# Kernel tuning notes

Measured on AMD Instinct MI355X. Metric: run time of the kernel, lower is better.

The kernel has to match this reference:

```python
import jax, jax.numpy as jnp
import numpy as np

B, SEQ, DIM = 4, 2048, 2048
NH, HD = 16, 128            # head_dim = dim // n_head
HID = 5632                  # int(2*(4*dim)/3) rounded up to multiple_of=256
EPS = 1e-5
THETA = 500000.0


def setup_inputs() -> dict:
    key = jax.random.key(0)
    ks = jax.random.split(key, 9)
    s = 0.02  # init scale keeps activations/logits well-conditioned
    x = jax.random.normal(ks[0], (B, SEQ, DIM), jnp.float32)
    wq = jax.random.normal(ks[1], (DIM, DIM), jnp.float32) * s
    wk = jax.random.normal(ks[2], (DIM, DIM), jnp.float32) * s
    wv = jax.random.normal(ks[3], (DIM, DIM), jnp.float32) * s
    wo = jax.random.normal(ks[4], (DIM, DIM), jnp.float32) * s
    w1 = jax.random.normal(ks[5], (DIM, HID), jnp.float32) * s
    w2 = jax.random.normal(ks[6], (HID, DIM), jnp.float32) * s
    w3 = jax.random.normal(ks[7], (DIM, HID), jnp.float32) * s
    attn_norm_w = jnp.ones((DIM,), jnp.float32)
    ffn_norm_w = jnp.ones((DIM,), jnp.float32)
    # RoPE tables (real/imag of freqs_cis), [seq, head_dim//2]
    inv = 1.0 / (THETA ** (jnp.arange(0, HD, 2, dtype=jnp.float32) / HD))
    ang = jnp.arange(SEQ, dtype=jnp.float32)[:, None] * inv[None, :]
    return dict(x=x, wq=wq, wk=wk, wv=wv, wo=wo, w1=w1, w2=w2, w3=w3,
                attn_norm_w=attn_norm_w, ffn_norm_w=ffn_norm_w,
                freqs_cos=jnp.cos(ang), freqs_sin=jnp.sin(ang))


def rmsnorm(x, w, eps=EPS):
    return x * jax.lax.rsqrt(jnp.mean(x * x, axis=-1, keepdims=True) + eps) * w


def rope(x, cos, sin):
    # x: [b, s, h, d]; pairs (d0,d1),(d2,d3),... treated as complex, multiplied by e^{i*ang}
    a, b = x[..., 0::2], x[..., 1::2]
    c = cos[None, :, None, :]
    s = sin[None, :, None, :]
    return jnp.stack([a * c - b * s, a * s + b * c], axis=-1).reshape(x.shape)


def block(x, wq, wk, wv, wo, w1, w2, w3, attn_norm_w, ffn_norm_w, freqs_cos, freqs_sin):
    b, s, d = x.shape
    # --- attention sublayer ---
    hn = rmsnorm(x, attn_norm_w)
    q = (hn @ wq).reshape(b, s, NH, HD)
    k = (hn @ wk).reshape(b, s, NH, HD)
    v = (hn @ wv).reshape(b, s, NH, HD)
    q = rope(q, freqs_cos, freqs_sin)
    k = rope(k, freqs_cos, freqs_sin)
    scores = jnp.einsum('bqhd,bkhd->bhqk', q, k) / np.float32(np.sqrt(HD))
    mask = jnp.triu(jnp.full((s, s), -jnp.inf, dtype=scores.dtype), k=1)
    p = jax.nn.softmax(scores + mask, axis=-1)
    attn = jnp.einsum('bhqk,bkhd->bqhd', p, v).reshape(b, s, d) @ wo
    h = x + attn
    # --- SwiGLU FFN sublayer ---
    fn = rmsnorm(h, ffn_norm_w)
    ffn = (jax.nn.silu(fn @ w1) * (fn @ w3)) @ w2
    return h + ffn


def reference(x, wq, wk, wv, wo, w1, w2, w3, attn_norm_w, ffn_norm_w, freqs_cos, freqs_sin):
    return block(x, wq, wk, wv, wo, w1, w2, w3, attn_norm_w, ffn_norm_w, freqs_cos, freqs_sin)
```

## Files before the change

### kernel.cpp

```cpp
#include <hip/hip_runtime.h>
#include <stdint.h>

#define DIMV 2048
#define SEQV 2048
#define NHV 16
#define HDV 128
#define HIDV 5632
#define NROWS 8192
#define LDP 6144

typedef short bf16x8 __attribute__((ext_vector_type(8)));
typedef float f32x4 __attribute__((ext_vector_type(4)));
typedef unsigned short u16x8 __attribute__((ext_vector_type(8)));

#define GLD16(src, dst) __builtin_amdgcn_global_load_lds( \
    (const __attribute__((address_space(1))) unsigned int*)(src), \
    (__attribute__((address_space(3))) unsigned int*)(dst), 16, 0, 0)

__device__ __forceinline__ float bf2f(unsigned short u){
  union { unsigned u; float f; } x; x.u = ((unsigned)u) << 16; return x.f;
}
__device__ __forceinline__ unsigned short f2bf(float f){
  union { float f; unsigned u; } x; x.f = f;
  unsigned r = x.u + 0x7fffu + ((x.u >> 16) & 1u);
  return (unsigned short)(r >> 16);
}

__global__ void transpose_cast(const float* __restrict__ in, unsigned short* __restrict__ out,
                               int R, int C){
  __shared__ alignas(16) unsigned short tile[32][33];
  int c0 = blockIdx.x * 32, r0 = blockIdx.y * 32;
  int tx = threadIdx.x, ty = threadIdx.y;
#pragma unroll
  for (int i = 0; i < 32; i += 8)
    tile[ty + i][tx] = f2bf(in[(long)(r0 + ty + i) * C + (c0 + tx)]);
  __syncthreads();
#pragma unroll
  for (int i = 0; i < 32; i += 8)
    out[(long)(c0 + ty + i) * R + (r0 + tx)] = tile[tx][ty + i];
}

__global__ void transpose_v(const unsigned short* __restrict__ packed, unsigned short* __restrict__ vt){
  __shared__ alignas(16) unsigned short tile[32][33];
  int bh = blockIdx.z;
  int b = bh >> 4, h = bh & 15;
  int d0 = blockIdx.y * 32, s0 = blockIdx.x * 32;
  int tx = threadIdx.x, ty = threadIdx.y;
  const unsigned short* src = packed + (long)b * SEQV * LDP + 4096 + (long)h * HDV;
  unsigned short* dst = vt + (long)bh * HDV * SEQV;
#pragma unroll
  for (int i = 0; i < 32; i += 8)
    tile[ty + i][tx] = src[(long)(s0 + ty + i) * LDP + d0 + tx];
  __syncthreads();
#pragma unroll
  for (int i = 0; i < 32; i += 8)
    dst[(long)(d0 + ty + i) * SEQV + s0 + tx] = tile[tx][ty + i];
}

__global__ __launch_bounds__(256) void rmsnorm_k(const float* __restrict__ x,
                                                 const float* __restrict__ w,
                                                 unsigned short* __restrict__ out){
  int row = blockIdx.x, t = threadIdx.x;
  const float* xr = x + (long)row * DIMV;
  float4 v0 = ((const float4*)xr)[t * 2];
  float4 v1 = ((const float4*)xr)[t * 2 + 1];
  float ss = v0.x*v0.x + v0.y*v0.y + v0.z*v0.z + v0.w*v0.w
           + v1.x*v1.x + v1.y*v1.y + v1.z*v1.z + v1.w*v1.w;
#pragma unroll
  for (int off = 32; off; off >>= 1) ss += __shfl_down(ss, off);
  __shared__ float red[4];
  if ((t & 63) == 0) red[t >> 6] = ss;
  __syncthreads();
  float tot = red[0] + red[1] + red[2] + red[3];
  float sc = rsqrtf(tot * (1.0f / DIMV) + 1e-5f);
  const float* wr = w + t * 8;
  float vv[8] = {v0.x, v0.y, v0.z, v0.w, v1.x, v1.y, v1.z, v1.w};
  u16x8 o;
#pragma unroll
  for (int e = 0; e < 8; e++) o[e] = f2bf(vv[e] * sc * wr[e]);
  *(u16x8*)(out + (long)row * DIMV + t * 8) = o;
}

template <int MODE>
__global__ __launch_bounds__(512, 2) void gemm256(const unsigned short* __restrict__ A, int lda,
                                                  const unsigned short* __restrict__ Bt,
                                                  unsigned short* __restrict__ Cb,
                                                  float* __restrict__ Cf,
                                                  const float* __restrict__ resid,
                                                  int ldc, int M, int N, int K){
  __shared__ alignas(16) unsigned short As[2][256 * 64];
  __shared__ alignas(16) unsigned short Bs[2][256 * 64];
  int m0 = blockIdx.y * 256, n0 = blockIdx.x * 256;
  int tid = threadIdx.x, w = tid >> 6, l = tid & 63;
  int wm = w >> 2, wn = w & 3;
  int l15 = l & 15, l4 = l >> 4;
  int sr8 = l >> 3, sl = l & 7;
  int nt = K / 64;

  f32x4 acc[8][4];
#pragma unroll
  for (int i = 0; i < 8; i++)
#pragma unroll
    for (int j = 0; j < 4; j++) acc[i][j] = (f32x4){0.f, 0.f, 0.f, 0.f};

#define GSTAGE(Gp, ld_, r0_, slab) { \
    _Pragma("unroll") \
    for (int r = 0; r < 2; r++){ \
      int row = (r * 8 + w) * 8 + sr8; \
      int cs = sl ^ (row & 7); \
      GLD16((Gp) + (long)((r0_) + row) * (ld_) + cs * 8, (slab) + (r * 8 + w) * 512); \
    } }
#define STAGE_A(tt, half) { int _t = (tt); if (_t < nt) GSTAGE(A + _t * 64, lda, m0 + (half) * 128, &As[_t & 1][(half) * 8192]) }
#define STAGE_B(tt, half) { int _t = (tt); if (_t < nt) GSTAGE(Bt + _t * 64, K, n0 + (half) * 128, &Bs[_t & 1][(half) * 8192]) }
#define LDA8(mi, ks) (*(const bf16x8*)(&As[bi][(wm * 128 + (mi) * 16 + l15) * 64 + (((ks) * 4 + l4) ^ (l15 & 7)) * 8]))
#define LDB8(ni, ks) (*(const bf16x8*)(&Bs[bi][(wn * 64 + (ni) * 16 + l15) * 64 + (((ks) * 4 + l4) ^ (l15 & 7)) * 8]))

  STAGE_A(0, 0); STAGE_A(0, 1); STAGE_B(0, 0); STAGE_B(0, 1);
  STAGE_A(1, 0); STAGE_B(1, 0); STAGE_B(1, 1);
  asm volatile("s_waitcnt vmcnt(6)" ::: "memory");
  __syncthreads();

  for (int t = 0; t < nt; t++){
    int bi = t & 1;
    bf16x8 af[8][2], bf0[2][2], bf1[2][2];
#pragma unroll
    for (int mi = 0; mi < 8; mi++){ af[mi][0] = LDA8(mi, 0); af[mi][1] = LDA8(mi, 1); }
#pragma unroll
    for (int ni = 0; ni < 2; ni++){ bf0[ni][0] = LDB8(ni, 0); bf0[ni][1] = LDB8(ni, 1); }
    STAGE_A(t + 1, 1);
    __builtin_amdgcn_s_barrier();
    asm volatile("s_waitcnt lgkmcnt(0)" ::: "memory");
    __builtin_amdgcn_sched_barrier(0);
    __builtin_amdgcn_s_setprio(1);
#pragma unroll
    for (int mi = 0; mi < 4; mi++)
#pragma unroll
      for (int ni = 0; ni < 2; ni++)
#pragma unroll
        for (int ks = 0; ks < 2; ks++)
          acc[mi][ni] = __builtin_amdgcn_mfma_f32_16x16x32_bf16(af[mi][ks], bf0[ni][ks], acc[mi][ni], 0, 0, 0);
    __builtin_amdgcn_s_setprio(0);
    __builtin_amdgcn_s_barrier();
#pragma unroll
    for (int ni = 0; ni < 2; ni++){ bf1[ni][0] = LDB8(ni + 2, 0); bf1[ni][1] = LDB8(ni + 2, 1); }
    STAGE_A(t + 2, 0);
    __builtin_amdgcn_s_barrier();
    asm volatile("s_waitcnt lgkmcnt(0)" ::: "memory");
    __builtin_amdgcn_sched_barrier(0);
    __builtin_amdgcn_s_setprio(1);
#pragma unroll
    for (int mi = 4; mi < 8; mi++)
#pragma unroll
      for (int ni = 0; ni < 2; ni++)
#pragma unroll
        for (int ks = 0; ks < 2; ks++)
          acc[mi][ni] = __builtin_amdgcn_mfma_f32_16x16x32_bf16(af[mi][ks], bf0[ni][ks], acc[mi][ni], 0, 0, 0);
    __builtin_amdgcn_s_setprio(0);
    __builtin_amdgcn_s_barrier();
    STAGE_B(t + 2, 0);
    __builtin_amdgcn_s_barrier();
    __builtin_amdgcn_s_setprio(1);
#pragma unroll
    for (int mi = 0; mi < 4; mi++)
#pragma unroll
      for (int ni = 0; ni < 2; ni++)
#pragma unroll
        for (int ks = 0; ks < 2; ks++)
          acc[mi][ni + 2] = __builtin_amdgcn_mfma_f32_16x16x32_bf16(af[mi][ks], bf1[ni][ks], acc[mi][ni + 2], 0, 0, 0);
    __builtin_amdgcn_s_setprio(0);
    __builtin_amdgcn_s_barrier();
    STAGE_B(t + 2, 1);
    __builtin_amdgcn_s_barrier();
    __builtin_amdgcn_s_setprio(1);
#pragma unroll
    for (int mi = 4; mi < 8; mi++)
#pragma unroll
      for (int ni = 0; ni < 2; ni++)
#pragma unroll
        for (int ks = 0; ks < 2; ks++)
          acc[mi][ni + 2] = __builtin_amdgcn_mfma_f32_16x16x32_bf16(af[mi][ks], bf1[ni][ks], acc[mi][ni + 2], 0, 0, 0);
    __builtin_amdgcn_s_setprio(0);
    if (t + 2 < nt) asm volatile("s_waitcnt vmcnt(6)" ::: "memory");
    else            asm volatile("s_waitcnt vmcnt(0)" ::: "memory");
    __builtin_amdgcn_s_barrier();
  }
#undef GSTAGE
#undef STAGE_A
#undef STAGE_B
#undef LDA8
#undef LDB8

#pragma unroll
  for (int mi = 0; mi < 8; mi++)
#pragma unroll
    for (int ni = 0; ni < 4; ni++)
#pragma unroll
      for (int r = 0; r < 4; r++){
        int row = m0 + wm * 128 + mi * 16 + l4 * 4 + r;
        int col = n0 + wn * 64 + ni * 16 + l15;
        long idx = (long)row * ldc + col;
        float v = acc[mi][ni][r];
        if (MODE == 0) Cb[idx] = f2bf(v);
        else           Cf[idx] = v + resid[idx];
      }
}

__global__ __launch_bounds__(512, 2) void ffn13_256(const unsigned short* __restrict__ A,
                                                    const unsigned short* __restrict__ B1t,
                                                    const unsigned short* __restrict__ B3t,
                                                    unsigned short* __restrict__ G,
                                                    int M, int N, int K){
  __shared__ alignas(16) unsigned short As[2][256 * 64];
  __shared__ alignas(16) unsigned short B1s[2][128 * 64];
  __shared__ alignas(16) unsigned short B3s[2][128 * 64];
  int m0 = blockIdx.y * 256, n0 = blockIdx.x * 128;
  int tid = threadIdx.x, w = tid >> 6, l = tid & 63;
  int wm = w >> 2, wn = w & 3;
  int l15 = l & 15, l4 = l >> 4;
  int sr8 = l >> 3, sl = l & 7;
  int nt = K / 64;

  f32x4 acc1[8][2], acc3[8][2];
#pragma unroll
  for (int i = 0; i < 8; i++)
#pragma unroll
    for (int j = 0; j < 2; j++){ acc1[i][j] = (f32x4){0.f,0.f,0.f,0.f}; acc3[i][j] = (f32x4){0.f,0.f,0.f,0.f}; }

#define GSTAGE(Gp, ld_, r0_, slab) { \
    _Pragma("unroll") \
    for (int r = 0; r < 2; r++){ \
      int row = (r * 8 + w) * 8 + sr8; \
      int cs = sl ^ (row & 7); \
      GLD16((Gp) + (long)((r0_) + row) * (ld_) + cs * 8, (slab) + (r * 8 + w) * 512); \
    } }
#define STAGE_A(tt, half) { int _t = (tt); if (_t < nt) GSTAGE(A + _t * 64, K, m0 + (half) * 128, &As[_t & 1][(half) * 8192]) }
#define STAGE_B1(tt) { int _t = (tt); if (_t < nt) GSTAGE(B1t + _t * 64, K, n0, &B1s[_t & 1][0]) }
#define STAGE_B3(tt) { int _t = (tt); if (_t < nt) GSTAGE(B3t + _t * 64, K, n0, &B3s[_t & 1][0]) }
#define LDA8(mi, ks) (*(const bf16x8*)(&As[bi][(wm * 128 + (mi) * 16 + l15) * 64 + (((ks) * 4 + l4) ^ (l15 & 7)) * 8]))
#define LDB18(ni, ks) (*(const bf16x8*)(&B1s[bi][(wn * 32 + (ni) * 16 + l15) * 64 + (((ks) * 4 + l4) ^ (l15 & 7)) * 8]))
#define LDB38(ni, ks) (*(const bf16x8*)(&B3s[bi][(wn * 32 + (ni) * 16 + l15) * 64 + (((ks) * 4 + l4) ^ (l15 & 7)) * 8]))

  STAGE_A(0, 0); STAGE_A(0, 1); STAGE_B1(0); STAGE_B3(0);
  STAGE_A(1, 0); STAGE_B1(1); STAGE_B3(1);
  asm volatile("s_waitcnt vmcnt(6)" ::: "memory");
  __syncthreads();

  for (int t = 0; t < nt; t++){
    int bi = t & 1;
    bf16x8 af[8][2], b1f[2][2], b3f[2][2];
#pragma unroll
    for (int mi = 0; mi < 8; mi++){ af[mi][0] = LDA8(mi, 0); af[mi][1] = LDA8(mi, 1); }
#pragma unroll
    for (int ni = 0; ni < 2; ni++){ b1f[ni][0] = LDB18(ni, 0); b1f[ni][1] = LDB18(ni, 1); }
    STAGE_A(t + 1, 1);
    __builtin_amdgcn_s_barrier();
    asm volatile("s_waitcnt lgkmcnt(0)" ::: "memory");
    __builtin_amdgcn_sched_barrier(0);
    __builtin_amdgcn_s_setprio(1);
#pragma unroll
    for (int mi = 0; mi < 4; mi++)
#pragma unroll
      for (int ni = 0; ni < 2; ni++)
#pragma unroll
        for (int ks = 0; ks < 2; ks++)
          acc1[mi][ni] = __builtin_amdgcn_mfma_f32_16x16x32_bf16(af[mi][ks], b1f[ni][ks], acc1[mi][ni], 0, 0, 0);
    __builtin_amdgcn_s_setprio(0);
    __builtin_amdgcn_s_barrier();
#pragma unroll
    for (int ni = 0; ni < 2; ni++){ b3f[ni][0] = LDB38(ni, 0); b3f[ni][1] = LDB38(ni, 1); }
    STAGE_A(t + 2, 0);
    __builtin_amdgcn_s_barrier();
    asm volatile("s_waitcnt lgkmcnt(0)" ::: "memory");
    __builtin_amdgcn_sched_barrier(0);
    __builtin_amdgcn_s_setprio(1);
#pragma unroll
    for (int mi = 4; mi < 8; mi++)
#pragma unroll
      for (int ni = 0; ni < 2; ni++)
#pragma unroll
        for (int ks = 0; ks < 2; ks++)
          acc1[mi][ni] = __builtin_amdgcn_mfma_f32_16x16x32_bf16(af[mi][ks], b1f[ni][ks], acc1[mi][ni], 0, 0, 0);
    __builtin_amdgcn_s_setprio(0);
    __builtin_amdgcn_s_barrier();
    STAGE_B1(t + 2);
    __builtin_amdgcn_s_barrier();
    __builtin_amdgcn_s_setprio(1);
#pragma unroll
    for (int mi = 0; mi < 4; mi++)
#pragma unroll
      for (int ni = 0; ni < 2; ni++)
#pragma unroll
        for (int ks = 0; ks < 2; ks++)
          acc3[mi][ni] = __builtin_amdgcn_mfma_f32_16x16x32_bf16(af[mi][ks], b3f[ni][ks], acc3[mi][ni], 0, 0, 0);
    __builtin_amdgcn_s_setprio(0);
    __builtin_amdgcn_s_barrier();
    STAGE_B3(t + 2);
    __builtin_amdgcn_s_barrier();
    __builtin_amdgcn_s_setprio(1);
#pragma unroll
    for (int mi = 4; mi < 8; mi++)
#pragma unroll
      for (int ni = 0; ni < 2; ni++)
#pragma unroll
        for (int ks = 0; ks < 2; ks++)
          acc3[mi][ni] = __builtin_amdgcn_mfma_f32_16x16x32_bf16(af[mi][ks], b3f[ni][ks], acc3[mi][ni], 0, 0, 0);
    __builtin_amdgcn_s_setprio(0);
    if (t + 2 < nt) asm volatile("s_waitcnt vmcnt(6)" ::: "memory");
    else            asm volatile("s_waitcnt vmcnt(0)" ::: "memory");
    __builtin_amdgcn_s_barrier();
  }
#undef GSTAGE
#undef STAGE_A
#undef STAGE_B1
#undef STAGE_B3
#undef LDA8
#undef LDB18
#undef LDB38

#pragma unroll
  for (int mi = 0; mi < 8; mi++)
#pragma unroll
    for (int ni = 0; ni < 2; ni++)
#pragma unroll
      for (int r = 0; r < 4; r++){
        int row = m0 + wm * 128 + mi * 16 + l4 * 4 + r;
        int col = n0 + wn * 32 + ni * 16 + l15;
        float a = acc1[mi][ni][r];
        float si = a * (1.f / (1.f + __expf(-a)));
        G[(long)row * N + col] = f2bf(si * acc3[mi][ni][r]);
      }
}

__global__ __launch_bounds__(256) void rope_k(unsigned short* __restrict__ p,
                                              const float* __restrict__ cosT,
                                              const float* __restrict__ sinT,
                                              float qscale){
  long idx = (long)blockIdx.x * 256 + threadIdx.x;
  int i = (int)(idx & 63);
  long t = idx >> 6;
  int h = (int)(t & 15);
  long row = t >> 4;
  int s = (int)(row & (SEQV - 1));
  float c = cosT[s * 64 + i], sn = sinT[s * 64 + i];
  long base = row * LDP + h * HDV + 2 * i;
  unsigned pq = *(unsigned*)(p + base);
  float a = bf2f((unsigned short)(pq & 0xffff)), b = bf2f((unsigned short)(pq >> 16));
  float ra = (a * c - b * sn) * qscale, rb = (a * sn + b * c) * qscale;
  *(unsigned*)(p + base) = (unsigned)f2bf(ra) | ((unsigned)f2bf(rb) << 16);
  unsigned pk = *(unsigned*)(p + base + 2048);
  a = bf2f((unsigned short)(pk & 0xffff)); b = bf2f((unsigned short)(pk >> 16));
  ra = a * c - b * sn; rb = a * sn + b * c;
  *(unsigned*)(p + base + 2048) = (unsigned)f2bf(ra) | ((unsigned)f2bf(rb) << 16);
}

__global__ __launch_bounds__(256) void attn_k(unsigned short* __restrict__ p,
                                              const unsigned short* __restrict__ vt){
  __shared__ alignas(16) unsigned short Ks[2][64 * 128];
  __shared__ alignas(16) unsigned short Vs[2][128 * 64];
  __shared__ alignas(16) unsigned short Ps[4][16 * 64];
  int qt = (gridDim.x - 1) - blockIdx.x;
  int bh = blockIdx.y;
  int b = bh >> 4, h = bh & 15;
  int tid = threadIdx.x, w = tid >> 6, l = tid & 63;
  int l15 = l & 15, l4 = l >> 4;
  int qrow0 = qt * 64 + w * 16;
  long baseQ = (long)b * SEQV * LDP + (long)h * HDV;
  long baseV = (long)bh * HDV * SEQV;

  bf16x8 qf[4];
#pragma unroll
  for (int dc = 0; dc < 4; dc++)
    qf[dc] = *(const bf16x8*)(p + baseQ + (long)(qrow0 + l15) * LDP + dc * 32 + l4 * 8);

  f32x4 acc[8];
#pragma unroll
  for (int df = 0; df < 8; df++) acc[df] = (f32x4){0.f, 0.f, 0.f, 0.f};
  float mOld[4], lsum[4];
#pragma unroll
  for (int r = 0; r < 4; r++){ mOld[r] = -1e30f; lsum[r] = 0.f; }

#define ATTN_STAGE(buf, kt) {                                                       \
    int k0 = (kt) * 64;                                                             \
    _Pragma("unroll")                                                               \
    for (int i = 0; i < 4; i++){                                                    \
      int row = w * 16 + i * 4 + (l >> 4);                                          \
      int slot = (l & 15) ^ (row & 7);                                              \
      GLD16(p + baseQ + 2048 + (long)(k0 + row) * LDP + slot * 8,                   \
            Ks[buf] + (w * 16 + i * 4) * 128);                                      \
    }                                                                               \
    _Pragma("unroll")                                                               \
    for (int i = 0; i < 4; i++){                                                    \
      int row = w * 32 + i * 8 + (l >> 3);                                          \
      int slot = (l & 7) ^ (row & 7);                                               \
      GLD16(vt + baseV + (long)row * SEQV + k0 + slot * 8,                          \
            Vs[buf] + (w * 32 + i * 8) * 64);                                       \
    } }

  int ntile = qt + 1;
  ATTN_STAGE(0, 0);
  asm volatile("s_waitcnt vmcnt(0)" ::: "memory");
  __syncthreads();
  int cur = 0;
  for (int tki = 0; tki < ntile; tki++){
    int k0 = tki * 64;
    if (tki + 1 < ntile) ATTN_STAGE(cur ^ 1, tki + 1);

    float s[4][4];
    __builtin_amdgcn_s_setprio(1);
#pragma unroll
    for (int kf = 0; kf < 4; kf++){
      f32x4 sf = (f32x4){0.f, 0.f, 0.f, 0.f};
#pragma unroll
      for (int dc = 0; dc < 4; dc++){
        bf16x8 kb = *(const bf16x8*)(Ks[cur] + (kf * 16 + l15) * 128 + (((dc * 4 + l4) ^ (l15 & 7)) * 8));
        sf = __builtin_amdgcn_mfma_f32_16x16x32_bf16(qf[dc], kb, sf, 0, 0, 0);
      }
      int key = k0 + kf * 16 + l15;
#pragma unroll
      for (int r = 0; r < 4; r++){
        int rowi = qrow0 + l4 * 4 + r;
        s[kf][r] = (key <= rowi) ? sf[r] : -1e30f;
      }
    }
    __builtin_amdgcn_s_setprio(0);
    float scale[4];
#pragma unroll
    for (int r = 0; r < 4; r++){
      float vmax = fmaxf(fmaxf(s[0][r], s[1][r]), fmaxf(s[2][r], s[3][r]));
      for (int mm = 8; mm; mm >>= 1) vmax = fmaxf(vmax, __shfl_xor(vmax, mm));
      float mNew = fmaxf(mOld[r], vmax);
      scale[r] = __expf(mOld[r] - mNew);
      float ps = 0.f;
#pragma unroll
      for (int kf = 0; kf < 4; kf++){
        float pp = __expf(s[kf][r] - mNew);
        s[kf][r] = pp;
        ps += pp;
      }
      for (int mm = 8; mm; mm >>= 1) ps += __shfl_xor(ps, mm);
      lsum[r] = lsum[r] * scale[r] + ps;
      mOld[r] = mNew;
    }
#pragma unroll
    for (int df = 0; df < 8; df++)
#pragma unroll
      for (int r = 0; r < 4; r++) acc[df][r] *= scale[r];
#pragma unroll
    for (int kf = 0; kf < 4; kf++)
#pragma unroll
      for (int r = 0; r < 4; r++){
        int row = l4 * 4 + r;
        int sidx = row * 64 + (((((kf * 16 + l15) * 2)) ^ ((row & 7) << 4)) >> 1);
        Ps[w][sidx] = f2bf(s[kf][r]);
      }
    __builtin_amdgcn_s_setprio(1);
#pragma unroll
    for (int kc = 0; kc < 2; kc++){
      bf16x8 pa = *(const bf16x8*)(Ps[w] + l15 * 64 + (((kc * 64 + l4 * 16) ^ ((l15 & 7) << 4)) >> 1));
#pragma unroll
      for (int df = 0; df < 8; df++){
        bf16x8 vb = *(const bf16x8*)(Vs[cur] + (df * 16 + l15) * 64 + (((kc * 4 + l4) ^ (l15 & 7)) * 8));
        acc[df] = __builtin_amdgcn_mfma_f32_16x16x32_bf16(pa, vb, acc[df], 0, 0, 0);
      }
    }
    __builtin_amdgcn_s_setprio(0);
    asm volatile("s_waitcnt vmcnt(0)" ::: "memory");
    __syncthreads();
    cur ^= 1;
  }
#pragma unroll
  for (int df = 0; df < 8; df++)
#pragma unroll
    for (int r = 0; r < 4; r++){
      int rows = qrow0 + l4 * 4 + r;
      p[baseQ + (long)rows * LDP + df * 16 + l15] = f2bf(acc[df][r] / lsum[r]);
    }
#undef ATTN_STAGE
}

extern "C" void kernel_launch(void* const* d_in, const int* in_sizes, int n_in,
                              void* d_out, int out_size, void* d_ws, size_t ws_size,
                              hipStream_t stream){
  const float* x    = (const float*)d_in[0];
  const float* wq   = (const float*)d_in[1];
  const float* wk   = (const float*)d_in[2];
  const float* wv   = (const float*)d_in[3];
  const float* wo   = (const float*)d_in[4];
  const float* w1   = (const float*)d_in[5];
  const float* w2   = (const float*)d_in[6];
  const float* w3   = (const float*)d_in[7];
  const float* anw  = (const float*)d_in[8];
  const float* fnw  = (const float*)d_in[9];
  const float* fcos = (const float*)d_in[10];
  const float* fsin = (const float*)d_in[11];

  char* ws = (char*)d_ws;
  size_t off = 0;
  auto alloc = [&](size_t bytes) -> void* {
    void* p = ws + off;
    off += (bytes + 255) & ~(size_t)255;
    return p;
  };
  const size_t SQ = (size_t)DIMV * DIMV * 2;
  const size_t SW = (size_t)DIMV * HIDV * 2;
  const size_t SA = (size_t)NROWS * DIMV * 2;
  const size_t SP = (size_t)NROWS * LDP * 2;

  unsigned short* wqT = (unsigned short*)alloc(SQ);
  unsigned short* wkT = (unsigned short*)alloc(SQ);
  unsigned short* wvT = (unsigned short*)alloc(SQ);
  unsigned short* woT = (unsigned short*)alloc(SQ);
  unsigned short* w1T = (unsigned short*)alloc(SW);
  unsigned short* w3T = (unsigned short*)alloc(SW);
  unsigned short* w2T = (unsigned short*)alloc(SW);
  unsigned short* hn  = (unsigned short*)alloc(SA);
  unsigned short* pk  = (unsigned short*)alloc(SP);
  unsigned short* vtb = hn;
  unsigned short* g   = pk;
  float* hf = (float*)d_out;
  (void)ws_size; (void)in_sizes; (void)n_in; (void)out_size;
  (void)wkT; (void)wvT;

  dim3 tb(32, 8);
  transpose_cast<<<dim3(DIMV/32, DIMV/32), tb, 0, stream>>>(wq, wqT, DIMV, DIMV);
  transpose_cast<<<dim3(DIMV/32, DIMV/32), tb, 0, stream>>>(wk, wkT, DIMV, DIMV);
  transpose_cast<<<dim3(DIMV/32, DIMV/32), tb, 0, stream>>>(wv, wvT, DIMV, DIMV);
  transpose_cast<<<dim3(DIMV/32, DIMV/32), tb, 0, stream>>>(wo, woT, DIMV, DIMV);
  transpose_cast<<<dim3(HIDV/32, DIMV/32), tb, 0, stream>>>(w1, w1T, DIMV, HIDV);
  transpose_cast<<<dim3(HIDV/32, DIMV/32), tb, 0, stream>>>(w3, w3T, DIMV, HIDV);
  transpose_cast<<<dim3(DIMV/32, HIDV/32), tb, 0, stream>>>(w2, w2T, HIDV, DIMV);

  rmsnorm_k<<<NROWS, 256, 0, stream>>>(x, anw, hn);

  gemm256<0><<<dim3(LDP/256, NROWS/256), 512, 0, stream>>>(hn, DIMV, wqT, pk, nullptr, nullptr, LDP, NROWS, LDP, DIMV);

  rope_k<<<(NROWS * NHV * 64) / 256, 256, 0, stream>>>(pk, fcos, fsin, 0.08838834764831845f);

  transpose_v<<<dim3(SEQV/32, HDV/32, 4 * NHV), tb, 0, stream>>>(pk, vtb);

  attn_k<<<dim3(SEQV/64, 4 * NHV), 256, 0, stream>>>(pk, vtb);

  gemm256<1><<<dim3(DIMV/256, NROWS/256), 512, 0, stream>>>(pk, LDP, woT, nullptr, hf, x, DIMV, NROWS, DIMV, DIMV);

  rmsnorm_k<<<NROWS, 256, 0, stream>>>(hf, fnw, hn);

  ffn13_256<<<dim3(HIDV/128, NROWS/256), 512, 0, stream>>>(hn, w1T, w3T, g, NROWS, HIDV, DIMV);

  gemm256<1><<<dim3(DIMV/256, NROWS/256), 512, 0, stream>>>(g, HIDV, w2T, nullptr, hf, (const float*)hf, DIMV, NROWS, DIMV, HIDV);
}
```

Measured before the change: 1.276 ms.

## Software-pipeline LDS fragment reads against MFMA quadrants in GEMM kernels

In both the generic 256x256 GEMM and the fused FFN w1/w3 kernel, the A fragments are split into two halves and the B fragments into two pairs. Each half is loaded from LDS just before the MFMA quadrant that needs it. The first quadrant's fragments for the next k-tile are prefetched while the last quadrant's MFMAs run, and the explicit lgkmcnt(0) waits are removed. The goal is to hide LDS read latency behind matrix-core work instead of stalling before each compute phase. This adds more scheduling barriers, and correctness now relies on the compiler inserting the LDS waits.

```diff
diff --git a/kernel.cpp b/kernel.cpp
--- a/kernel.cpp
+++ b/kernel.cpp
@@ -80,6 +80,9 @@
   for (int e = 0; e < 8; e++) o[e] = f2bf(vv[e] * sc * wr[e]);
   *(u16x8*)(out + (long)row * DIMV + t * 8) = o;
 }
+
+#define SCHEDB() __builtin_amdgcn_sched_barrier(0)
+#define SBAR()   __builtin_amdgcn_s_barrier()
 
 template <int MODE>
 __global__ __launch_bounds__(512, 2) void gemm256(const unsigned short* __restrict__ A, int lda,
@@ -112,83 +115,79 @@
     } }
 #define STAGE_A(tt, half) { int _t = (tt); if (_t < nt) GSTAGE(A + _t * 64, lda, m0 + (half) * 128, &As[_t & 1][(half) * 8192]) }
 #define STAGE_B(tt, half) { int _t = (tt); if (_t < nt) GSTAGE(Bt + _t * 64, K, n0 + (half) * 128, &Bs[_t & 1][(half) * 8192]) }
-#define LDA8(mi, ks) (*(const bf16x8*)(&As[bi][(wm * 128 + (mi) * 16 + l15) * 64 + (((ks) * 4 + l4) ^ (l15 & 7)) * 8]))
-#define LDB8(ni, ks) (*(const bf16x8*)(&Bs[bi][(wn * 64 + (ni) * 16 + l15) * 64 + (((ks) * 4 + l4) ^ (l15 & 7)) * 8]))
+#define LDA8(bb, mi, ks) (*(const bf16x8*)(&As[bb][(wm * 128 + (mi) * 16 + l15) * 64 + (((ks) * 4 + l4) ^ (l15 & 7)) * 8]))
+#define LDB8(bb, ni, ks) (*(const bf16x8*)(&Bs[bb][(wn * 64 + (ni) * 16 + l15) * 64 + (((ks) * 4 + l4) ^ (l15 & 7)) * 8]))
+#define Q_MFMA(AF, BF, MOFF, NOFF) { \
+    _Pragma("unroll") \
+    for (int mi = 0; mi < 4; mi++) \
+      _Pragma("unroll") \
+      for (int ni = 0; ni < 2; ni++) \
+        _Pragma("unroll") \
+        for (int ks = 0; ks < 2; ks++) \
+          acc[mi + (MOFF)][ni + (NOFF)] = __builtin_amdgcn_mfma_f32_16x16x32_bf16(AF[mi][ks], BF[ni][ks], acc[mi + (MOFF)][ni + (NOFF)], 0, 0, 0); }
+
+  bf16x8 a03[4][2], a47[4][2], b01[2][2], b23[2][2];
 
   STAGE_A(0, 0); STAGE_A(0, 1); STAGE_B(0, 0); STAGE_B(0, 1);
   STAGE_A(1, 0); STAGE_B(1, 0); STAGE_B(1, 1);
   asm volatile("s_waitcnt vmcnt(6)" ::: "memory");
-  __syncthreads();
+  SBAR();
+  SCHEDB();
+#pragma unroll
+  for (int mi = 0; mi < 4; mi++){ a03[mi][0] = LDA8(0, mi, 0); a03[mi][1] = LDA8(0, mi, 1); }
+#pragma unroll
+  for (int ni = 0; ni < 2; ni++){ b01[ni][0] = LDB8(0, ni, 0); b01[ni][1] = LDB8(0, ni, 1); }
+  SCHEDB();
 
   for (int t = 0; t < nt; t++){
     int bi = t & 1;
-    bf16x8 af[8][2], bf0[2][2], bf1[2][2];
-#pragma unroll
-    for (int mi = 0; mi < 8; mi++){ af[mi][0] = LDA8(mi, 0); af[mi][1] = LDA8(mi, 1); }
-#pragma unroll
-    for (int ni = 0; ni < 2; ni++){ bf0[ni][0] = LDB8(ni, 0); bf0[ni][1] = LDB8(ni, 1); }
+#pragma unroll
+    for (int mi = 0; mi < 4; mi++){ a47[mi][0] = LDA8(bi, mi + 4, 0); a47[mi][1] = LDA8(bi, mi + 4, 1); }
     STAGE_A(t + 1, 1);
-    __builtin_amdgcn_s_barrier();
-    asm volatile("s_waitcnt lgkmcnt(0)" ::: "memory");
-    __builtin_amdgcn_sched_barrier(0);
-    __builtin_amdgcn_s_setprio(1);
-#pragma unroll
-    for (int mi = 0; mi < 4; mi++)
-#pragma unroll
-      for (int ni = 0; ni < 2; ni++)
-#pragma unroll
-        for (int ks = 0; ks < 2; ks++)
-          acc[mi][ni] = __builtin_amdgcn_mfma_f32_16x16x32_bf16(af[mi][ks], bf0[ni][ks], acc[mi][ni], 0, 0, 0);
-    __builtin_amdgcn_s_setprio(0);
-    __builtin_amdgcn_s_barrier();
-#pragma unroll
-    for (int ni = 0; ni < 2; ni++){ bf1[ni][0] = LDB8(ni + 2, 0); bf1[ni][1] = LDB8(ni + 2, 1); }
+    SCHEDB(); SBAR(); SCHEDB();
+    __builtin_amdgcn_s_setprio(1);
+    Q_MFMA(a03, b01, 0, 0);
+    __builtin_amdgcn_s_setprio(0);
+    SCHEDB(); SBAR();
+#pragma unroll
+    for (int ni = 0; ni < 2; ni++){ b23[ni][0] = LDB8(bi, ni + 2, 0); b23[ni][1] = LDB8(bi, ni + 2, 1); }
     STAGE_A(t + 2, 0);
-    __builtin_amdgcn_s_barrier();
-    asm volatile("s_waitcnt lgkmcnt(0)" ::: "memory");
-    __builtin_amdgcn_sched_barrier(0);
-    __builtin_amdgcn_s_setprio(1);
-#pragma unroll
-    for (int mi = 4; mi < 8; mi++)
-#pragma unroll
-      for (int ni = 0; ni < 2; ni++)
-#pragma unroll
-        for (int ks = 0; ks < 2; ks++)
-          acc[mi][ni] = __builtin_amdgcn_mfma_f32_16x16x32_bf16(af[mi][ks], bf0[ni][ks], acc[mi][ni], 0, 0, 0);
-    __builtin_amdgcn_s_setprio(0);
-    __builtin_amdgcn_s_barrier();
+    SCHEDB(); SBAR(); SCHEDB();
+    __builtin_amdgcn_s_setprio(1);
+    Q_MFMA(a47, b01, 4, 0);
+    __builtin_amdgcn_s_setprio(0);
+    SCHEDB(); SBAR();
     STAGE_B(t + 2, 0);
-    __builtin_amdgcn_s_barrier();
-    __builtin_amdgcn_s_setprio(1);
-#pragma unroll
-    for (int mi = 0; mi < 4; mi++)
-#pragma unroll
-      for (int ni = 0; ni < 2; ni++)
-#pragma unroll
-        for (int ks = 0; ks < 2; ks++)
-          acc[mi][ni + 2] = __builtin_amdgcn_mfma_f32_16x16x32_bf16(af[mi][ks], bf1[ni][ks], acc[mi][ni + 2], 0, 0, 0);
-    __builtin_amdgcn_s_setprio(0);
-    __builtin_amdgcn_s_barrier();
+    SCHEDB(); SBAR(); SCHEDB();
+    __builtin_amdgcn_s_setprio(1);
+    Q_MFMA(a03, b23, 0, 2);
+    __builtin_amdgcn_s_setprio(0);
+    SCHEDB(); SBAR();
     STAGE_B(t + 2, 1);
-    __builtin_amdgcn_s_barrier();
-    __builtin_amdgcn_s_setprio(1);
-#pragma unroll
-    for (int mi = 4; mi < 8; mi++)
-#pragma unroll
-      for (int ni = 0; ni < 2; ni++)
-#pragma unroll
-        for (int ks = 0; ks < 2; ks++)
-          acc[mi][ni + 2] = __builtin_amdgcn_mfma_f32_16x16x32_bf16(af[mi][ks], bf1[ni][ks], acc[mi][ni + 2], 0, 0, 0);
-    __builtin_amdgcn_s_setprio(0);
+    SCHEDB();
     if (t + 2 < nt) asm volatile("s_waitcnt vmcnt(6)" ::: "memory");
     else            asm volatile("s_waitcnt vmcnt(0)" ::: "memory");
-    __builtin_amdgcn_s_barrier();
+    SBAR();
+    SCHEDB();
+    if (t + 1 < nt){
+      int bj = bi ^ 1;
+#pragma unroll
+      for (int mi = 0; mi < 4; mi++){ a03[mi][0] = LDA8(bj, mi, 0); a03[mi][1] = LDA8(bj, mi, 1); }
+#pragma unroll
+      for (int ni = 0; ni < 2; ni++){ b01[ni][0] = LDB8(bj, ni, 0); b01[ni][1] = LDB8(bj, ni, 1); }
+    }
+    SCHEDB();
+    __builtin_amdgcn_s_setprio(1);
+    Q_MFMA(a47, b23, 4, 2);
+    __builtin_amdgcn_s_setprio(0);
+    SCHEDB(); SBAR();
   }
 #undef GSTAGE
 #undef STAGE_A
 #undef STAGE_B
 #undef LDA8
 #undef LDB8
+#undef Q_MFMA
 
 #pragma unroll
   for (int mi = 0; mi < 8; mi++)
@@ -236,78 +235,73 @@
 #define STAGE_A(tt, half) { int _t = (tt); if (_t < nt) GSTAGE(A + _t * 64, K, m0 + (half) * 128, &As[_t & 1][(half) * 8192]) }
 #define STAGE_B1(tt) { int _t = (tt); if (_t < nt) GSTAGE(B1t + _t * 64, K, n0, &B1s[_t & 1][0]) }
 #define STAGE_B3(tt) { int _t = (tt); if (_t < nt) GSTAGE(B3t + _t * 64, K, n0, &B3s[_t & 1][0]) }
-#define LDA8(mi, ks) (*(const bf16x8*)(&As[bi][(wm * 128 + (mi) * 16 + l15) * 64 + (((ks) * 4 + l4) ^ (l15 & 7)) * 8]))
-#define LDB18(ni, ks) (*(const bf16x8*)(&B1s[bi][(wn * 32 + (ni) * 16 + l15) * 64 + (((ks) * 4 + l4) ^ (l15 & 7)) * 8]))
-#define LDB38(ni, ks) (*(const bf16x8*)(&B3s[bi][(wn * 32 + (ni) * 16 + l15) * 64 + (((ks) * 4 + l4) ^ (l15 & 7)) * 8]))
+#define LDA8(bb, mi, ks) (*(const bf16x8*)(&As[bb][(wm * 128 + (mi) * 16 + l15) * 64 + (((ks) * 4 + l4) ^ (l15 & 7)) * 8]))
+#define LDB18(bb, ni, ks) (*(const bf16x8*)(&B1s[bb][(wn * 32 + (ni) * 16 + l15) * 64 + (((ks) * 4 + l4) ^ (l15 & 7)) * 8]))
+#define LDB38(bb, ni, ks) (*(const bf16x8*)(&B3s[bb][(wn * 32 + (ni) * 16 + l15) * 64 + (((ks) * 4 + l4) ^ (l15 & 7)) * 8]))
+#define Q_MFMA(AF, BF, ACC, MOFF) { \
+    _Pragma("unroll") \
+    for (int mi = 0; mi < 4; mi++) \
+      _Pragma("unroll") \
+      for (int ni = 0; ni < 2; ni++) \
+        _Pragma("unroll") \
+        for (int ks = 0; ks < 2; ks++) \
+          ACC[mi + (MOFF)][ni] = __builtin_amdgcn_mfma_f32_16x16x32_bf16(AF[mi][ks], BF[ni][ks], ACC[mi + (MOFF)][ni], 0, 0, 0); }
+
+  bf16x8 a03[4][2], a47[4][2], b1f[2][2], b3f[2][2];
 
   STAGE_A(0, 0); STAGE_A(0, 1); STAGE_B1(0); STAGE_B3(0);
   STAGE_A(1, 0); STAGE_B1(1); STAGE_B3(1);
   asm volatile("s_waitcnt vmcnt(6)" ::: "memory");
-  __syncthreads();
+  SBAR();
+  SCHEDB();
+#pragma unroll
+  for (int mi = 0; mi < 4; mi++){ a03[mi][0] = LDA8(0, mi, 0); a03[mi][1] = LDA8(0, mi, 1); }
+#pragma unroll
+  for (int ni = 0; ni < 2; ni++){ b1f[ni][0] = LDB18(0, ni, 0); b1f[ni][1] = LDB18(0, ni, 1); }
+  SCHEDB();
 
   for (int t = 0; t < nt; t++){
     int bi = t & 1;
-    bf16x8 af[8][2], b1f[2][2], b3f[2][2];
-#pragma unroll
-    for (int mi = 0; mi < 8; mi++){ af[mi][0] = LDA8(mi, 0); af[mi][1] = LDA8(mi, 1); }
-#pragma unroll
-    for (int ni = 0; ni < 2; ni++){ b1f[ni][0] = LDB18(ni, 0); b1f[ni][1] = LDB18(ni, 1); }
+#pragma unroll
+    for (int mi = 0; mi < 4; mi++){ a47[mi][0] = LDA8(bi, mi + 4, 0); a47[mi][1] = LDA8(bi, mi + 4, 1); }
     STAGE_A(t + 1, 1);
-    __builtin_amdgcn_s_barrier();
-    asm volatile("s_waitcnt lgkmcnt(0)" ::: "memory");
-    __builtin_amdgcn_sched_barrier(0);
-    __builtin_amdgcn_s_setprio(1);
-#pragma unroll
-    for (int mi = 0; mi < 4; mi++)
-#pragma unroll
-      for (int ni = 0; ni < 2; ni++)
-#pragma unroll
-        for (int ks = 0; ks < 2; ks++)
-          acc1[mi][ni] = __builtin_amdgcn_mfma_f32_16x16x32_bf16(af[mi][ks], b1f[ni][ks], acc1[mi][ni], 0, 0, 0);
-    __builtin_amdgcn_s_setprio(0);
-    __builtin_amdgcn_s_barrier();
-#pragma unroll
-    for (int ni = 0; ni < 2; ni++){ b3f[ni][0] = LDB38(ni, 0); b3f[ni][1] = LDB38(ni, 1); }
+    SCHEDB(); SBAR(); SCHEDB();
+    __builtin_amdgcn_s_setprio(1);
+    Q_MFMA(a03, b1f, acc1, 0);
+    __builtin_amdgcn_s_setprio(0);
+    SCHEDB(); SBAR();
+#pragma unroll
+    for (int ni = 0; ni < 2; ni++){ b3f[ni][0] = LDB38(bi, ni, 0); b3f[ni][1] = LDB38(bi, ni, 1); }
     STAGE_A(t + 2, 0);
-    __builtin_amdgcn_s_barrier();
-    asm volatile("s_waitcnt lgkmcnt(0)" ::: "memory");
-    __builtin_amdgcn_sched_barrier(0);
-    __builtin_amdgcn_s_setprio(1);
-#pragma unroll
-    for (int mi = 4; mi < 8; mi++)
-#pragma unroll
-      for (int ni = 0; ni < 2; ni++)
-#pragma unroll
-        for (int ks = 0; ks < 2; ks++)
-          acc1[mi][ni] = __builtin_amdgcn_mfma_f32_16x16x32_bf16(af[mi][ks], b1f[ni][ks], acc1[mi][ni], 0, 0, 0);
-    __builtin_amdgcn_s_setprio(0);
-    __builtin_amdgcn_s_barrier();
+    SCHEDB(); SBAR(); SCHEDB();
+    __builtin_amdgcn_s_setprio(1);
+    Q_MFMA(a47, b1f, acc1, 4);
+    __builtin_amdgcn_s_setprio(0);
+    SCHEDB(); SBAR();
     STAGE_B1(t + 2);
-    __builtin_amdgcn_s_barrier();
-    __builtin_amdgcn_s_setprio(1);
-#pragma unroll
-    for (int mi = 0; mi < 4; mi++)
-#pragma unroll
-      for (int ni = 0; ni < 2; ni++)
-#pragma unroll
-        for (int ks = 0; ks < 2; ks++)
-          acc3[mi][ni] = __builtin_amdgcn_mfma_f32_16x16x32_bf16(af[mi][ks], b3f[ni][ks], acc3[mi][ni], 0, 0, 0);
-    __builtin_amdgcn_s_setprio(0);
-    __builtin_amdgcn_s_barrier();
+    SCHEDB(); SBAR(); SCHEDB();
+    __builtin_amdgcn_s_setprio(1);
+    Q_MFMA(a03, b3f, acc3, 0);
+    __builtin_amdgcn_s_setprio(0);
+    SCHEDB(); SBAR();
     STAGE_B3(t + 2);
-    __builtin_amdgcn_s_barrier();
-    __builtin_amdgcn_s_setprio(1);
-#pragma unroll
-    for (int mi = 4; mi < 8; mi++)
-#pragma unroll
-      for (int ni = 0; ni < 2; ni++)
-#pragma unroll
-        for (int ks = 0; ks < 2; ks++)
-          acc3[mi][ni] = __builtin_amdgcn_mfma_f32_16x16x32_bf16(af[mi][ks], b3f[ni][ks], acc3[mi][ni], 0, 0, 0);
-    __builtin_amdgcn_s_setprio(0);
+    SCHEDB();
     if (t + 2 < nt) asm volatile("s_waitcnt vmcnt(6)" ::: "memory");
     else            asm volatile("s_waitcnt vmcnt(0)" ::: "memory");
-    __builtin_amdgcn_s_barrier();
+    SBAR();
+    SCHEDB();
+    if (t + 1 < nt){
+      int bj = bi ^ 1;
+#pragma unroll
+      for (int mi = 0; mi < 4; mi++){ a03[mi][0] = LDA8(bj, mi, 0); a03[mi][1] = LDA8(bj, mi, 1); }
+#pragma unroll
+      for (int ni = 0; ni < 2; ni++){ b1f[ni][0] = LDB18(bj, ni, 0); b1f[ni][1] = LDB18(bj, ni, 1); }
+    }
+    SCHEDB();
+    __builtin_amdgcn_s_setprio(1);
+    Q_MFMA(a47, b3f, acc3, 4);
+    __builtin_amdgcn_s_setprio(0);
+    SCHEDB(); SBAR();
   }
 #undef GSTAGE
 #undef STAGE_A
@@ -316,6 +310,7 @@
 #undef LDA8
 #undef LDB18
 #undef LDB38
+#undef Q_MFMA
 
 #pragma unroll
   for (int mi = 0; mi < 8; mi++)
```

Result: slower. 1.503 ms (+17.7%).
